# Optimization experiments

Hardware: AMD Instinct MI355X
Metric: run time of the kernel (lower is better)

The kernel has to match this reference:

```python
import jax, jax.numpy as jnp
import numpy as np

ALPHA = 0.1
K_STEPS = 10


def _with_self_loops(edge_index, n):
    loops = jnp.arange(n, dtype=edge_index.dtype)
    src = jnp.concatenate([edge_index[0], loops])
    dst = jnp.concatenate([edge_index[1], loops])
    return src, dst


def _gcn_norm(src, dst, n, dtype):
    # symmetric normalization deg^{-1/2}[src] * deg^{-1/2}[dst], deg over in-edges (incl. self loops)
    deg = jax.ops.segment_sum(jnp.ones(dst.shape[0], dtype=dtype), dst, num_segments=n)
    dinv = jnp.where(deg > 0, jax.lax.rsqrt(deg), jnp.zeros_like(deg))
    return dinv[src] * dinv[dst]


def _propagate(h, src, dst, norm, n):
    # gather -> scale -> scatter-add (A_hat @ h)
    msg = h[src] * norm[:, None]            # [E, d]
    return jax.ops.segment_sum(msg, dst, num_segments=n)


def setup_inputs() -> dict:
    key = jax.random.key(0)
    ks = jax.random.split(key, 8)
    N, E, D, H, C = 100000, 3200000, 256, 256, 40
    s = 1.0 / np.sqrt(D)
    return {
        "x": jax.random.normal(ks[0], (N, D), dtype=jnp.float32),
        "edge_index": jax.random.randint(ks[1], (2, E), 0, N, dtype=jnp.int64),
        "w1": jax.random.normal(ks[2], (D, H), dtype=jnp.float32) * s,
        "b1": jnp.zeros((H,), dtype=jnp.float32),
        "w2": jax.random.normal(ks[3], (H, H), dtype=jnp.float32) * s,
        "b2": jnp.zeros((H,), dtype=jnp.float32),
        "w3": jax.random.normal(ks[4], (H, H), dtype=jnp.float32) * s,
        "b3": jnp.zeros((H,), dtype=jnp.float32),
        "fc_w": jax.random.normal(ks[5], (H, C), dtype=jnp.float32) * s,
        "fc_b": jnp.zeros((C,), dtype=jnp.float32),
    }


def reference(x, edge_index, w1, b1, w2, b2, w3, b3, fc_w, fc_b):
    n = x.shape[0]
    src, dst = _with_self_loops(edge_index, n)
    norm = _gcn_norm(src, dst, n, x.dtype)

    def gcn_conv(h, w, b):
        h = h @ w                             # linear transform first (PyG GCNConv)
        return _propagate(h, src, dst, norm, n) + b

    h = jax.nn.relu(gcn_conv(x, w1, b1))
    h = jax.nn.relu(gcn_conv(h, w2, b2))
    h = jax.nn.relu(gcn_conv(h, w3, b3))      # convx with layer=3 has one extra GCNConv

    # APPNP: K steps of h <- (1-alpha) * A_hat h + alpha * h0
    h0 = h
    def step(h, _):
        h = (1.0 - ALPHA) * _propagate(h, src, dst, norm, n) + ALPHA * h0
        return h, None
    h, _ = jax.lax.scan(step, h, None, length=K_STEPS)

    logits = h @ fc_w + fc_b
    return jax.nn.log_softmax(logits, axis=1)
```

## Files before the change

### kernel.cpp

```cpp
#include <hip/hip_runtime.h>
#include <math.h>


constexpr int D  = 256;
constexpr int C  = 40;
constexpr int ZP = 64;

typedef _Float16 h2v    __attribute__((ext_vector_type(2)));
typedef _Float16 h4     __attribute__((ext_vector_type(4)));
typedef _Float16 half8v __attribute__((ext_vector_type(8)));
typedef float    f32x4  __attribute__((ext_vector_type(4)));

struct __align__(8) EdgeCV { int c; float v; };


__global__ void k_count(const int* __restrict__ dst, int* __restrict__ cnt,
                        int* __restrict__ eslot, int E) {
    int e = blockIdx.x * blockDim.x + threadIdx.x;
    if (e < E) eslot[e] = atomicAdd(&cnt[dst[e]], 1);
}

__global__ void k_alloc_self(const int* __restrict__ cnt, int* __restrict__ startA,
                             int* __restrict__ cursor, float* __restrict__ dinv,
                             EdgeCV* __restrict__ edges, int N) {
    int i = blockIdx.x * blockDim.x + threadIdx.x;
    if (i < N) {
        int c = cnt[i];
        int s = atomicAdd(cursor, c + 1);
        startA[i] = s;
        float dv = rsqrtf((float)(c + 1));
        dinv[i] = dv;
        EdgeCV ev; ev.c = i; ev.v = dv * dv;
        edges[s + c] = ev;
    }
}

__global__ void k_fill(const int* __restrict__ src, const int* __restrict__ dst,
                       const int* __restrict__ startA, const int* __restrict__ eslot,
                       const float* __restrict__ dinv, EdgeCV* __restrict__ edges, int E) {
    int e = blockIdx.x * blockDim.x + threadIdx.x;
    if (e < E) {
        int s = src[e], d = dst[e];
        EdgeCV ev; ev.c = s; ev.v = dinv[s] * dinv[d];
        edges[startA[d] + eslot[e]] = ev;
    }
}


__global__ void k_transW(const float* __restrict__ W0, const float* __restrict__ W1,
                         const float* __restrict__ W2, _Float16* __restrict__ Wt) {
    int n = blockIdx.x;
    int w = blockIdx.y;
    int k = threadIdx.x;
    const float* W = (w == 0) ? W0 : (w == 1) ? W1 : W2;
    Wt[(size_t)w * 65536 + n * 256 + k] = (_Float16)W[k * 256 + n];
}


template <typename TIN, bool SLICED>
__global__ __launch_bounds__(256, 1) void k_gemm_mfma(const TIN* __restrict__ A,
                                                      const _Float16* __restrict__ Wt,
                                                      _Float16* __restrict__ Cout, int M) {
    __shared__ _Float16 wlds[256][72];
    const int tid  = threadIdx.x;
    const int lane = tid & 63;
    const int wave = tid >> 6;
    const int l15  = lane & 15;
    const int lk8  = (lane >> 4) * 8;
    const int rowbase = blockIdx.x * 128 + wave * 32;
    const size_t sliceN = (size_t)M * 64;

    half8v a[2][8];
    #pragma unroll
    for (int mt = 0; mt < 2; ++mt) {
        int row = rowbase + mt * 16 + l15;
        bool ok = row < M;
        const TIN* ap = A + (size_t)(ok ? row : 0) * D;
        #pragma unroll
        for (int kk = 0; kk < 8; ++kk) {
            half8v v;
            if constexpr (sizeof(TIN) == 2) {
                v = *(const half8v*)(ap + kk * 32 + lk8);
            } else {
                float4 f0 = *(const float4*)(ap + kk * 32 + lk8);
                float4 f1 = *(const float4*)(ap + kk * 32 + lk8 + 4);
                v[0] = (_Float16)f0.x; v[1] = (_Float16)f0.y;
                v[2] = (_Float16)f0.z; v[3] = (_Float16)f0.w;
                v[4] = (_Float16)f1.x; v[5] = (_Float16)f1.y;
                v[6] = (_Float16)f1.z; v[7] = (_Float16)f1.w;
            }
            if (!ok) {
                half8v zz = {0, 0, 0, 0, 0, 0, 0, 0};
                v = zz;
            }
            a[mt][kk] = v;
        }
    }

    f32x4 acc[2][16] = {};

    #pragma unroll
    for (int s = 0; s < 4; ++s) {
        {
            const half8v* srcp = (const half8v*)(Wt + (size_t)tid * D + s * 64);
            #pragma unroll
            for (int cc = 0; cc < 8; ++cc)
                *(half8v*)(&wlds[tid][cc * 8]) = srcp[cc];
        }
        __syncthreads();
        #pragma unroll
        for (int kf = 0; kf < 2; ++kf) {
            const int kk = s * 2 + kf;
            #pragma unroll
            for (int nt = 0; nt < 16; ++nt) {
                half8v b = *(const half8v*)(&wlds[nt * 16 + l15][kf * 32 + lk8]);
                acc[0][nt] = __builtin_amdgcn_mfma_f32_16x16x32_f16(a[0][kk], b, acc[0][nt], 0, 0, 0);
                acc[1][nt] = __builtin_amdgcn_mfma_f32_16x16x32_f16(a[1][kk], b, acc[1][nt], 0, 0, 0);
            }
        }
        __syncthreads();
    }

    const int r0 = (lane >> 4) * 4;
    #pragma unroll
    for (int mt = 0; mt < 2; ++mt) {
        #pragma unroll
        for (int r = 0; r < 4; ++r) {
            int row = rowbase + mt * 16 + r0 + r;
            if (row < M) {
                if constexpr (SLICED) {
                    #pragma unroll
                    for (int nt = 0; nt < 16; ++nt) {
                        int col = nt * 16 + l15;
                        Cout[(size_t)(col >> 6) * sliceN + (size_t)row * 64 + (col & 63)]
                            = (_Float16)acc[mt][nt][r];
                    }
                } else {
                    _Float16* crow = Cout + (size_t)row * D;
                    #pragma unroll
                    for (int nt = 0; nt < 16; ++nt)
                        crow[nt * 16 + l15] = (_Float16)acc[mt][nt][r];
                }
            }
        }
    }
}


__global__ __launch_bounds__(256) void k_spmm_sliced(const _Float16* __restrict__ t,
                                                     const int* __restrict__ startA,
                                                     const int* __restrict__ cnt,
                                                     const EdgeCV* __restrict__ edges,
                                                     const float* __restrict__ bias,
                                                     _Float16* __restrict__ out, int N) {
    int gid   = (int)((blockIdx.x * 256u + threadIdx.x) >> 6);
    int lane  = threadIdx.x & 63;
    int slice = blockIdx.y;
    if (gid >= N) return;
    int start = startA[gid], end = start + cnt[gid] + 1;
    const _Float16* ts = t + (size_t)slice * ((size_t)N * 64);
    float a[8];
    #pragma unroll
    for (int i = 0; i < 8; ++i) a[i] = 0.f;
    int e = start;
    for (; e + 7 < end; e += 8) {
        EdgeCV c[8];
        float x[8];
        #pragma unroll
        for (int i = 0; i < 8; ++i) c[i] = edges[e + i];
        #pragma unroll
        for (int i = 0; i < 8; ++i) x[i] = (float)ts[(size_t)c[i].c * 64 + lane];
        #pragma unroll
        for (int i = 0; i < 8; ++i) a[i] += c[i].v * x[i];
    }
    for (; e < end; ++e) {
        EdgeCV c0 = edges[e];
        a[0] += c0.v * (float)ts[(size_t)c0.c * 64 + lane];
    }
    float acc = ((a[0] + a[1]) + (a[2] + a[3])) + ((a[4] + a[5]) + (a[6] + a[7]));
    float b = bias[slice * 64 + lane];
    out[(size_t)gid * D + slice * 64 + lane] = (_Float16)fmaxf(acc + b, 0.f);
}


__global__ __launch_bounds__(256) void k_spmm_relu(const _Float16* __restrict__ h,
                                                   const int* __restrict__ startA,
                                                   const int* __restrict__ cnt,
                                                   const EdgeCV* __restrict__ edges,
                                                   const float* __restrict__ bias,
                                                   _Float16* __restrict__ out, int N) {
    int gid  = (int)((blockIdx.x * 256u + threadIdx.x) >> 6);
    int lane = threadIdx.x & 63;
    if (gid >= N) return;
    int start = startA[gid], end = start + cnt[gid] + 1;
    const h4* hp = (const h4*)h;
    float4 s0 = make_float4(0.f, 0.f, 0.f, 0.f);
    float4 s1 = make_float4(0.f, 0.f, 0.f, 0.f);
    float4 s2 = make_float4(0.f, 0.f, 0.f, 0.f);
    float4 s3 = make_float4(0.f, 0.f, 0.f, 0.f);
    int e = start;
    for (; e + 3 < end; e += 4) {
        EdgeCV c0 = edges[e],     c1 = edges[e + 1];
        EdgeCV c2 = edges[e + 2], c3 = edges[e + 3];
        h4 x0 = hp[(size_t)c0.c * 64 + lane];
        h4 x1 = hp[(size_t)c1.c * 64 + lane];
        h4 x2 = hp[(size_t)c2.c * 64 + lane];
        h4 x3 = hp[(size_t)c3.c * 64 + lane];
        s0.x += c0.v * (float)x0[0]; s0.y += c0.v * (float)x0[1];
        s0.z += c0.v * (float)x0[2]; s0.w += c0.v * (float)x0[3];
        s1.x += c1.v * (float)x1[0]; s1.y += c1.v * (float)x1[1];
        s1.z += c1.v * (float)x1[2]; s1.w += c1.v * (float)x1[3];
        s2.x += c2.v * (float)x2[0]; s2.y += c2.v * (float)x2[1];
        s2.z += c2.v * (float)x2[2]; s2.w += c2.v * (float)x2[3];
        s3.x += c3.v * (float)x3[0]; s3.y += c3.v * (float)x3[1];
        s3.z += c3.v * (float)x3[2]; s3.w += c3.v * (float)x3[3];
    }
    for (; e < end; ++e) {
        EdgeCV c0 = edges[e];
        h4 x0 = hp[(size_t)c0.c * 64 + lane];
        s0.x += c0.v * (float)x0[0]; s0.y += c0.v * (float)x0[1];
        s0.z += c0.v * (float)x0[2]; s0.w += c0.v * (float)x0[3];
    }
    float4 acc = make_float4(s0.x + s1.x + s2.x + s3.x,
                             s0.y + s1.y + s2.y + s3.y,
                             s0.z + s1.z + s2.z + s3.z,
                             s0.w + s1.w + s2.w + s3.w);
    float4 b = ((const float4*)bias)[lane];
    h4 o;
    o[0] = (_Float16)fmaxf(acc.x + b.x, 0.f);
    o[1] = (_Float16)fmaxf(acc.y + b.y, 0.f);
    o[2] = (_Float16)fmaxf(acc.z + b.z, 0.f);
    o[3] = (_Float16)fmaxf(acc.w + b.w, 0.f);
    ((h4*)out)[(size_t)gid * 64 + lane] = o;
}


__global__ __launch_bounds__(256) void k_z0(const _Float16* __restrict__ h,
                                            const float* __restrict__ fcw,
                                            _Float16* __restrict__ z0, int N) {
    __shared__ float ws[D * C];
    for (int i = threadIdx.x; i < D * C; i += 256) ws[i] = fcw[i];
    __syncthreads();
    int row = blockIdx.x * 256 + threadIdx.x;
    if (row >= N) return;
    float acc[C] = {};
    const half8v* hr = (const half8v*)(h + (size_t)row * D);
    for (int kq = 0; kq < 32; ++kq) {
        half8v v = hr[kq];
        #pragma unroll
        for (int j = 0; j < 8; ++j) {
            float hv = (float)v[j];
            #pragma unroll
            for (int c = 0; c < C; ++c) acc[c] += hv * ws[(kq * 8 + j) * C + c];
        }
    }
    h2v* zr = (h2v*)(z0 + (size_t)row * ZP);
    #pragma unroll
    for (int c = 0; c < 20; ++c) {
        h2v o; o[0] = (_Float16)acc[2 * c]; o[1] = (_Float16)acc[2 * c + 1];
        zr[c] = o;
    }
    h2v zz = {(_Float16)0.f, (_Float16)0.f};
    #pragma unroll
    for (int c = 20; c < 32; ++c) zr[c] = zz;
}


__global__ __launch_bounds__(256) void k_spmm40(const _Float16* __restrict__ z,
                                                const int* __restrict__ startA,
                                                const int* __restrict__ cnt,
                                                const EdgeCV* __restrict__ edges,
                                                const _Float16* __restrict__ z0,
                                                _Float16* __restrict__ out, int N) {
    int wid  = (int)((blockIdx.x * 256u + threadIdx.x) >> 6);
    int lane = threadIdx.x & 63;
    int p    = lane >> 5;
    int l5   = lane & 31;
    int row  = wid * 2 + p;
    if (row >= N) return;
    int start = startA[row], end = start + cnt[row] + 1;
    const h2v* zp = (const h2v*)z;
    float ax[8], ay[8];
    #pragma unroll
    for (int i = 0; i < 8; ++i) { ax[i] = 0.f; ay[i] = 0.f; }
    int e = start;
    for (; e + 7 < end; e += 8) {
        EdgeCV c[8];
        h2v x[8];
        #pragma unroll
        for (int i = 0; i < 8; ++i) c[i] = edges[e + i];
        #pragma unroll
        for (int i = 0; i < 8; ++i) x[i] = zp[(size_t)c[i].c * 32 + l5];
        #pragma unroll
        for (int i = 0; i < 8; ++i) {
            ax[i] += c[i].v * (float)x[i][0];
            ay[i] += c[i].v * (float)x[i][1];
        }
    }
    for (; e < end; ++e) {
        EdgeCV c0 = edges[e];
        h2v x0 = zp[(size_t)c0.c * 32 + l5];
        ax[0] += c0.v * (float)x0[0]; ay[0] += c0.v * (float)x0[1];
    }
    float axs = ((ax[0] + ax[1]) + (ax[2] + ax[3])) + ((ax[4] + ax[5]) + (ax[6] + ax[7]));
    float ays = ((ay[0] + ay[1]) + (ay[2] + ay[3])) + ((ay[4] + ay[5]) + (ay[6] + ay[7]));
    h2v zz = ((const h2v*)z0)[(size_t)row * 32 + l5];
    axs = 0.9f * axs + 0.1f * (float)zz[0];
    ays = 0.9f * ays + 0.1f * (float)zz[1];
    h2v o; o[0] = (_Float16)axs; o[1] = (_Float16)ays;
    ((h2v*)out)[(size_t)row * 32 + l5] = o;
}


__global__ __launch_bounds__(256) void k_logsm(const _Float16* __restrict__ z,
                                               const float* __restrict__ fcb,
                                               float* __restrict__ out, int N) {
    __shared__ float bs[C];
    for (int i = threadIdx.x; i < C; i += 256) bs[i] = fcb[i];
    __syncthreads();
    int row = blockIdx.x * 256 + threadIdx.x;
    if (row >= N) return;
    float v[C];
    const h2v* zr = (const h2v*)(z + (size_t)row * ZP);
    #pragma unroll
    for (int c = 0; c < 20; ++c) {
        h2v t = zr[c];
        v[2 * c]     = (float)t[0] + bs[2 * c];
        v[2 * c + 1] = (float)t[1] + bs[2 * c + 1];
    }
    float m = v[0];
    #pragma unroll
    for (int c = 1; c < C; ++c) m = fmaxf(m, v[c]);
    float s = 0.f;
    #pragma unroll
    for (int c = 0; c < C; ++c) s += expf(v[c] - m);
    float lse = logf(s) + m;
    float* orow = out + (size_t)row * C;
    #pragma unroll
    for (int c = 0; c < C; ++c) orow[c] = v[c] - lse;
}


extern "C" void kernel_launch(void* const* d_in, const int* in_sizes, int n_in,
                              void* d_out, int out_size, void* d_ws, size_t ws_size,
                              hipStream_t stream) {
    const float* x   = (const float*)d_in[0];
    const int*   ei  = (const int*)d_in[1];
    const float* w1  = (const float*)d_in[2];
    const float* b1  = (const float*)d_in[3];
    const float* w2  = (const float*)d_in[4];
    const float* b2  = (const float*)d_in[5];
    const float* w3  = (const float*)d_in[6];
    const float* b3  = (const float*)d_in[7];
    const float* fcw = (const float*)d_in[8];
    const float* fcb = (const float*)d_in[9];
    float* out = (float*)d_out;

    const int N = in_sizes[0] / D;
    const int E = in_sizes[1] / 2;
    const int* srcArr = ei;
    const int* dstArr = ei + E;

    char* wsp = (char*)d_ws;
    size_t off = 0;
    auto take = [&](size_t bytes) -> void* {
        void* p = wsp + off;
        off = (off + bytes + 255) & ~(size_t)255;
        return p;
    };
    int*       cnt    = (int*)take((size_t)N * 4);
    int*       startA = (int*)take((size_t)N * 4);
    int*       eslot  = (int*)take((size_t)E * 4);
    int*       cursor = (int*)take(256);
    float*     dinv   = (float*)take((size_t)N * 4);
    EdgeCV*    edges  = (EdgeCV*)take((size_t)(E + N) * 8);
    _Float16*  bufA   = (_Float16*)take((size_t)N * D * 2);
    _Float16*  bufB   = (_Float16*)take((size_t)N * D * 2);
    _Float16*  bufC   = (_Float16*)take((size_t)N * D * 2);
    _Float16*  Wt     = (_Float16*)take((size_t)3 * D * D * 2);
    _Float16*  z0w    = (_Float16*)take((size_t)N * ZP * 2);
    _Float16*  zA     = (_Float16*)take((size_t)N * ZP * 2);
    _Float16*  zB     = (_Float16*)take((size_t)N * ZP * 2);
    (void)ws_size;

    dim3 b256(256);
    int gN = (N + 255) / 256;
    int gE = (E + 255) / 256;

    hipMemsetAsync(cursor, 0, 4, stream);
    hipMemsetAsync(cnt, 0, (size_t)N * 4, stream);
    k_count<<<gE, b256, 0, stream>>>(dstArr, cnt, eslot, E);
    k_alloc_self<<<gN, b256, 0, stream>>>(cnt, startA, cursor, dinv, edges, N);
    k_fill<<<gE, b256, 0, stream>>>(srcArr, dstArr, startA, eslot, dinv, edges, E);

    dim3 tg(256, 3);
    k_transW<<<tg, b256, 0, stream>>>(w1, w2, w3, Wt);

    dim3 gg((N + 127) / 128);
    int spBlocks   = (N + 3) / 4;
    int sp40Blocks = (N + 7) / 8;
    dim3 slicedGrid((N + 3) / 4, 4);

    k_gemm_mfma<float, true><<<gg, b256, 0, stream>>>(x, Wt, bufB, N);
    k_spmm_sliced<<<slicedGrid, b256, 0, stream>>>(bufB, startA, cnt, edges, b1, bufA, N);
    k_gemm_mfma<_Float16, false><<<gg, b256, 0, stream>>>(bufA, Wt + 65536, bufB, N);
    k_spmm_relu<<<spBlocks, b256, 0, stream>>>(bufB, startA, cnt, edges, b2, bufA, N);
    k_gemm_mfma<_Float16, false><<<gg, b256, 0, stream>>>(bufA, Wt + 131072, bufB, N);
    k_spmm_relu<<<spBlocks, b256, 0, stream>>>(bufB, startA, cnt, edges, b3, bufC, N);

    k_z0<<<gN, b256, 0, stream>>>(bufC, fcw, z0w, N);

    const _Float16* zc = z0w;
    _Float16* zn = zA;
    for (int it = 0; it < 10; ++it) {
        k_spmm40<<<sp40Blocks, b256, 0, stream>>>(zc, startA, cnt, edges, z0w, zn, N);
        zc = zn;
        zn = (zn == zA) ? zB : zA;
    }

    k_logsm<<<gN, b256, 0, stream>>>(zc, fcb, out, N);
}
```

Measured before the change: 2.115 ms.

## Compute z0 projection with MFMA and drop sliced layer-1 SpMM

Replaces the scalar per-row fc projection kernel, which staged fc_w in shared memory and kept 40 fp32 accumulators per thread, with an MFMA kernel that uses a transposed, zero-padded fp16 fc weight. z0 is now memset to zero beforehand so its padding columns stay clean. The first layer also drops the 4-slice column-partitioned GEMM output and SpMM, using the row-major GEMM and the standard vectorized SpMM instead. The aim is to remove the slow scalar projection and the sliced gather pattern, at the cost of an extra memset and a small weight-transpose kernel.

```diff
diff --git a/kernel.cpp b/kernel.cpp
--- a/kernel.cpp
+++ b/kernel.cpp
@@ -56,8 +56,14 @@
     Wt[(size_t)w * 65536 + n * 256 + k] = (_Float16)W[k * 256 + n];
 }
 
-
-template <typename TIN, bool SLICED>
+__global__ void k_transFc(const float* __restrict__ fcw, _Float16* __restrict__ FcT) {
+    int n = blockIdx.x;
+    int k = threadIdx.x;
+    FcT[n * 256 + k] = (n < C) ? (_Float16)fcw[k * C + n] : (_Float16)0.f;
+}
+
+
+template <typename TIN>
 __global__ __launch_bounds__(256, 1) void k_gemm_mfma(const TIN* __restrict__ A,
                                                       const _Float16* __restrict__ Wt,
                                                       _Float16* __restrict__ Cout, int M) {
@@ -68,7 +74,6 @@
     const int l15  = lane & 15;
     const int lk8  = (lane >> 4) * 8;
     const int rowbase = blockIdx.x * 128 + wave * 32;
-    const size_t sliceN = (size_t)M * 64;
 
     half8v a[2][8];
     #pragma unroll
@@ -128,58 +133,67 @@
         for (int r = 0; r < 4; ++r) {
             int row = rowbase + mt * 16 + r0 + r;
             if (row < M) {
-                if constexpr (SLICED) {
-                    #pragma unroll
-                    for (int nt = 0; nt < 16; ++nt) {
-                        int col = nt * 16 + l15;
-                        Cout[(size_t)(col >> 6) * sliceN + (size_t)row * 64 + (col & 63)]
-                            = (_Float16)acc[mt][nt][r];
-                    }
-                } else {
-                    _Float16* crow = Cout + (size_t)row * D;
-                    #pragma unroll
-                    for (int nt = 0; nt < 16; ++nt)
-                        crow[nt * 16 + l15] = (_Float16)acc[mt][nt][r];
+                _Float16* crow = Cout + (size_t)row * D;
+                #pragma unroll
+                for (int nt = 0; nt < 16; ++nt)
+                    crow[nt * 16 + l15] = (_Float16)acc[mt][nt][r];
+            }
+        }
+    }
+}
+
+
+__global__ __launch_bounds__(256, 1) void k_z0_mfma(const _Float16* __restrict__ h,
+                                                    const _Float16* __restrict__ FcT,
+                                                    _Float16* __restrict__ z0, int M) {
+    const int tid  = threadIdx.x;
+    const int lane = tid & 63;
+    const int wave = tid >> 6;
+    const int l15  = lane & 15;
+    const int lk8  = (lane >> 4) * 8;
+    const int rowbase = blockIdx.x * 128 + wave * 32;
+
+    half8v a[2][8];
+    #pragma unroll
+    for (int mt = 0; mt < 2; ++mt) {
+        int row = rowbase + mt * 16 + l15;
+        bool ok = row < M;
+        const _Float16* ap = h + (size_t)(ok ? row : 0) * D;
+        #pragma unroll
+        for (int kk = 0; kk < 8; ++kk) {
+            half8v v = *(const half8v*)(ap + kk * 32 + lk8);
+            if (!ok) { half8v zz = {0,0,0,0,0,0,0,0}; v = zz; }
+            a[mt][kk] = v;
+        }
+    }
+
+    f32x4 acc[2][3] = {};
+    #pragma unroll
+    for (int kk = 0; kk < 8; ++kk) {
+        #pragma unroll
+        for (int nt = 0; nt < 3; ++nt) {
+            half8v b = *(const half8v*)(FcT + (size_t)(nt * 16 + l15) * D + kk * 32 + lk8);
+            acc[0][nt] = __builtin_amdgcn_mfma_f32_16x16x32_f16(a[0][kk], b, acc[0][nt], 0, 0, 0);
+            acc[1][nt] = __builtin_amdgcn_mfma_f32_16x16x32_f16(a[1][kk], b, acc[1][nt], 0, 0, 0);
+        }
+    }
+
+    const int r0 = (lane >> 4) * 4;
+    #pragma unroll
+    for (int mt = 0; mt < 2; ++mt) {
+        #pragma unroll
+        for (int r = 0; r < 4; ++r) {
+            int row = rowbase + mt * 16 + r0 + r;
+            if (row < M) {
+                _Float16* zrow = z0 + (size_t)row * ZP;
+                #pragma unroll
+                for (int nt = 0; nt < 3; ++nt) {
+                    int col = nt * 16 + l15;
+                    if (col < C) zrow[col] = (_Float16)acc[mt][nt][r];
                 }
             }
         }
     }
-}
-
-
-__global__ __launch_bounds__(256) void k_spmm_sliced(const _Float16* __restrict__ t,
-                                                     const int* __restrict__ startA,
-                                                     const int* __restrict__ cnt,
-                                                     const EdgeCV* __restrict__ edges,
-                                                     const float* __restrict__ bias,
-                                                     _Float16* __restrict__ out, int N) {
-    int gid   = (int)((blockIdx.x * 256u + threadIdx.x) >> 6);
-    int lane  = threadIdx.x & 63;
-    int slice = blockIdx.y;
-    if (gid >= N) return;
-    int start = startA[gid], end = start + cnt[gid] + 1;
-    const _Float16* ts = t + (size_t)slice * ((size_t)N * 64);
-    float a[8];
-    #pragma unroll
-    for (int i = 0; i < 8; ++i) a[i] = 0.f;
-    int e = start;
-    for (; e + 7 < end; e += 8) {
-        EdgeCV c[8];
-        float x[8];
-        #pragma unroll
-        for (int i = 0; i < 8; ++i) c[i] = edges[e + i];
-        #pragma unroll
-        for (int i = 0; i < 8; ++i) x[i] = (float)ts[(size_t)c[i].c * 64 + lane];
-        #pragma unroll
-        for (int i = 0; i < 8; ++i) a[i] += c[i].v * x[i];
-    }
-    for (; e < end; ++e) {
-        EdgeCV c0 = edges[e];
-        a[0] += c0.v * (float)ts[(size_t)c0.c * 64 + lane];
-    }
-    float acc = ((a[0] + a[1]) + (a[2] + a[3])) + ((a[4] + a[5]) + (a[6] + a[7]));
-    float b = bias[slice * 64 + lane];
-    out[(size_t)gid * D + slice * 64 + lane] = (_Float16)fmaxf(acc + b, 0.f);
 }
 
 
@@ -235,37 +249,6 @@
 }
 
 
-__global__ __launch_bounds__(256) void k_z0(const _Float16* __restrict__ h,
-                                            const float* __restrict__ fcw,
-                                            _Float16* __restrict__ z0, int N) {
-    __shared__ float ws[D * C];
-    for (int i = threadIdx.x; i < D * C; i += 256) ws[i] = fcw[i];
-    __syncthreads();
-    int row = blockIdx.x * 256 + threadIdx.x;
-    if (row >= N) return;
-    float acc[C] = {};
-    const half8v* hr = (const half8v*)(h + (size_t)row * D);
-    for (int kq = 0; kq < 32; ++kq) {
-        half8v v = hr[kq];
-        #pragma unroll
-        for (int j = 0; j < 8; ++j) {
-            float hv = (float)v[j];
-            #pragma unroll
-            for (int c = 0; c < C; ++c) acc[c] += hv * ws[(kq * 8 + j) * C + c];
-        }
-    }
-    h2v* zr = (h2v*)(z0 + (size_t)row * ZP);
-    #pragma unroll
-    for (int c = 0; c < 20; ++c) {
-        h2v o; o[0] = (_Float16)acc[2 * c]; o[1] = (_Float16)acc[2 * c + 1];
-        zr[c] = o;
-    }
-    h2v zz = {(_Float16)0.f, (_Float16)0.f};
-    #pragma unroll
-    for (int c = 20; c < 32; ++c) zr[c] = zz;
-}
-
-
 __global__ __launch_bounds__(256) void k_spmm40(const _Float16* __restrict__ z,
                                                 const int* __restrict__ startA,
                                                 const int* __restrict__ cnt,
@@ -378,6 +361,7 @@
     _Float16*  bufB   = (_Float16*)take((size_t)N * D * 2);
     _Float16*  bufC   = (_Float16*)take((size_t)N * D * 2);
     _Float16*  Wt     = (_Float16*)take((size_t)3 * D * D * 2);
+    _Float16*  FcT    = (_Float16*)take((size_t)48 * D * 2);
     _Float16*  z0w    = (_Float16*)take((size_t)N * ZP * 2);
     _Float16*  zA     = (_Float16*)take((size_t)N * ZP * 2);
     _Float16*  zB     = (_Float16*)take((size_t)N * ZP * 2);
@@ -389,26 +373,27 @@
 
     hipMemsetAsync(cursor, 0, 4, stream);
     hipMemsetAsync(cnt, 0, (size_t)N * 4, stream);
+    hipMemsetAsync(z0w, 0, (size_t)N * ZP * 2, stream);
     k_count<<<gE, b256, 0, stream>>>(dstArr, cnt, eslot, E);
     k_alloc_self<<<gN, b256, 0, stream>>>(cnt, startA, cursor, dinv, edges, N);
     k_fill<<<gE, b256, 0, stream>>>(srcArr, dstArr, startA, eslot, dinv, edges, E);
 
     dim3 tg(256, 3);
     k_transW<<<tg, b256, 0, stream>>>(w1, w2, w3, Wt);
+    k_transFc<<<48, b256, 0, stream>>>(fcw, FcT);
 
     dim3 gg((N + 127) / 128);
     int spBlocks   = (N + 3) / 4;
     int sp40Blocks = (N + 7) / 8;
-    dim3 slicedGrid((N + 3) / 4, 4);
-
-    k_gemm_mfma<float, true><<<gg, b256, 0, stream>>>(x, Wt, bufB, N);
-    k_spmm_sliced<<<slicedGrid, b256, 0, stream>>>(bufB, startA, cnt, edges, b1, bufA, N);
-    k_gemm_mfma<_Float16, false><<<gg, b256, 0, stream>>>(bufA, Wt + 65536, bufB, N);
+
+    k_gemm_mfma<float><<<gg, b256, 0, stream>>>(x, Wt, bufB, N);
+    k_spmm_relu<<<spBlocks, b256, 0, stream>>>(bufB, startA, cnt, edges, b1, bufA, N);
+    k_gemm_mfma<_Float16><<<gg, b256, 0, stream>>>(bufA, Wt + 65536, bufB, N);
     k_spmm_relu<<<spBlocks, b256, 0, stream>>>(bufB, startA, cnt, edges, b2, bufA, N);
-    k_gemm_mfma<_Float16, false><<<gg, b256, 0, stream>>>(bufA, Wt + 131072, bufB, N);
+    k_gemm_mfma<_Float16><<<gg, b256, 0, stream>>>(bufA, Wt + 131072, bufB, N);
     k_spmm_relu<<<spBlocks, b256, 0, stream>>>(bufB, startA, cnt, edges, b3, bufC, N);
 
-    k_z0<<<gN, b256, 0, stream>>>(bufC, fcw, z0w, N);
+    k_z0_mfma<<<gg, b256, 0, stream>>>(bufC, FcT, z0w, N);
 
     const _Float16* zc = z0w;
     _Float16* zn = zA;
```

Result: faster. 1.943 ms (-8.1%).
